# Kernel optimization log

Measured on AMD Instinct MI355X. Metric: run time of the kernel, lower is better.

Reference implementation:

```python
import jax, jax.numpy as jnp
import numpy as np

# class_mask_range after __init__ normalization: first range (-1,1) => min=-1, max=1,
# so the rescale 2*(x-min)/(max-min)-1 is the identity on all ranges.
RANGES = [(-1.0, 1.0), (-1.0, -0.5), (-0.5, 0.0), (0.0, 0.5), (0.5, 1.0)]
N_CLASSES = len(RANGES)
WEIGHTS = [1.0 / N_CLASSES] * N_CLASSES  # class_weight [1]*5 normalized by its sum


def setup_inputs() -> dict:
    key = jax.random.key(0)
    k1, k2 = jax.random.split(key)
    shape = (16, 1, 1024, 1024)
    return {
        "pre_img": jax.random.normal(k1, shape, dtype=jnp.float32),
        "real_img": jax.random.normal(k2, shape, dtype=jnp.float32),
    }


def reference(pre_img, real_img):
    # |pre*mask - real*mask| == mask * |pre - real| for 0/1 masks
    diff = jnp.abs(pre_img - real_img)
    class_mask = jnp.zeros(real_img.shape, dtype=jnp.int32)
    single_class_losses = []
    for i, (lb, ub) in enumerate(RANGES):
        m = (real_img >= lb) & (real_img <= ub)
        # later ranges overwrite earlier assignments, as in the torch loop
        class_mask = jnp.where(m, jnp.int32(i), class_mask)
        counts = m.sum()
        masked_sum = jnp.where(m, diff, 0.0).sum()
        denom = jnp.maximum(counts, 1).astype(diff.dtype)
        loss_i = jnp.where(counts == 0, 0.0, masked_sum / denom) * WEIGHTS[i]
        single_class_losses.append(loss_i)
    loss = sum(single_class_losses)
    class_mask_out = 2.0 * class_mask.astype(jnp.float32) / (N_CLASSES - 1) - 1.0
    return loss, jnp.stack(single_class_losses), class_mask_out
```

## Files before the change

### kernel.cpp

```cpp
#include <hip/hip_runtime.h>


__global__ __launch_bounds__(256) void mcl_main(
    const float* __restrict__ pre, const float* __restrict__ real,
    float* __restrict__ mask_out, float* __restrict__ sums,
    unsigned int* __restrict__ counts, int n4, int n)
{
    float s[5] = {0.f, 0.f, 0.f, 0.f, 0.f};
    unsigned int c[5] = {0u, 0u, 0u, 0u, 0u};

    const int tid = blockIdx.x * blockDim.x + threadIdx.x;
    const int stride = gridDim.x * blockDim.x;

    for (int i = tid; i < n4; i += stride) {
        float4 p = ((const float4*)pre)[i];
        float4 r = ((const float4*)real)[i];
        float pv[4] = {p.x, p.y, p.z, p.w};
        float rv[4] = {r.x, r.y, r.z, r.w};
        float ov[4];
#pragma unroll
        for (int k = 0; k < 4; ++k) {
            float rr = rv[k];
            float d = fabsf(pv[k] - rr);
            bool in0 = (rr >= -1.0f) && (rr <= 1.0f);
            bool in1 = (rr >= -1.0f) && (rr <= -0.5f);
            bool in2 = (rr >= -0.5f) && (rr <= 0.0f);
            bool in3 = (rr >= 0.0f) && (rr <= 0.5f);
            bool in4 = (rr >= 0.5f) && (rr <= 1.0f);
            s[0] += in0 ? d : 0.f; c[0] += in0;
            s[1] += in1 ? d : 0.f; c[1] += in1;
            s[2] += in2 ? d : 0.f; c[2] += in2;
            s[3] += in3 ? d : 0.f; c[3] += in3;
            s[4] += in4 ? d : 0.f; c[4] += in4;
            int cls = in4 ? 4 : (in3 ? 3 : (in2 ? 2 : (in1 ? 1 : 0)));
            ov[k] = 0.5f * (float)cls - 1.0f;
        }
        float2* mo = (float2*)(mask_out + 4 * (size_t)i);
        mo[0] = make_float2(ov[0], ov[1]);
        mo[1] = make_float2(ov[2], ov[3]);
    }

    int tail_base = n4 * 4;
    int tail = n - tail_base;
    if (tid < tail) {
        int idx = tail_base + tid;
        float rr = real[idx];
        float d = fabsf(pre[idx] - rr);
        bool in0 = (rr >= -1.0f) && (rr <= 1.0f);
        bool in1 = (rr >= -1.0f) && (rr <= -0.5f);
        bool in2 = (rr >= -0.5f) && (rr <= 0.0f);
        bool in3 = (rr >= 0.0f) && (rr <= 0.5f);
        bool in4 = (rr >= 0.5f) && (rr <= 1.0f);
        s[0] += in0 ? d : 0.f; c[0] += in0;
        s[1] += in1 ? d : 0.f; c[1] += in1;
        s[2] += in2 ? d : 0.f; c[2] += in2;
        s[3] += in3 ? d : 0.f; c[3] += in3;
        s[4] += in4 ? d : 0.f; c[4] += in4;
        int cls = in4 ? 4 : (in3 ? 3 : (in2 ? 2 : (in1 ? 1 : 0)));
        mask_out[idx] = 0.5f * (float)cls - 1.0f;
    }

#pragma unroll
    for (int j = 0; j < 5; ++j) {
#pragma unroll
        for (int off = 32; off > 0; off >>= 1) {
            s[j] += __shfl_down(s[j], off, 64);
            c[j] += __shfl_down(c[j], off, 64);
        }
    }

    __shared__ float ls[4][5];
    __shared__ unsigned int lc[4][5];
    int lane = threadIdx.x & 63;
    int wave = threadIdx.x >> 6;
    if (lane == 0) {
#pragma unroll
        for (int j = 0; j < 5; ++j) { ls[wave][j] = s[j]; lc[wave][j] = c[j]; }
    }
    __syncthreads();
    if (threadIdx.x < 5) {
        float ssum = ls[0][threadIdx.x] + ls[1][threadIdx.x]
                   + ls[2][threadIdx.x] + ls[3][threadIdx.x];
        unsigned int csum = lc[0][threadIdx.x] + lc[1][threadIdx.x]
                          + lc[2][threadIdx.x] + lc[3][threadIdx.x];
        atomicAdd(&sums[threadIdx.x], ssum);
        atomicAdd(&counts[threadIdx.x], csum);
    }
}

__global__ void mcl_final(const float* __restrict__ sums,
                          const unsigned int* __restrict__ counts,
                          float* __restrict__ out)
{
    if (threadIdx.x == 0) {
        float total = 0.f;
        float losses[5];
#pragma unroll
        for (int j = 0; j < 5; ++j) {
            unsigned int cnt = counts[j];
            unsigned int denom = cnt > 1u ? cnt : 1u;
            float l = (cnt == 0u) ? 0.f : (sums[j] / (float)denom) * 0.2f;
            losses[j] = l;
            total += l;
        }
        out[0] = total;
#pragma unroll
        for (int j = 0; j < 5; ++j) out[1 + j] = losses[j];
    }
}

extern "C" void kernel_launch(void* const* d_in, const int* in_sizes, int n_in,
                              void* d_out, int out_size, void* d_ws, size_t ws_size,
                              hipStream_t stream) {
    const float* pre  = (const float*)d_in[0];
    const float* real = (const float*)d_in[1];
    float* out = (float*)d_out;
    int n = in_sizes[0];
    int n4 = n / 4;

    float* sums = (float*)d_ws;
    unsigned int* counts = (unsigned int*)((char*)d_ws + 5 * sizeof(float));

    hipMemsetAsync(d_ws, 0, 10 * sizeof(float), stream);

    const int blocks = 1024;
    mcl_main<<<blocks, 256, 0, stream>>>(pre, real, out + 6, sums, counts, n4, n);
    mcl_final<<<1, 64, 0, stream>>>(sums, counts, out);
}
```

Baseline: 189.8 us.

## Launch one block per 512 float4s with two loads per thread and padded atomics

Replaces the fixed 1024-block grid-stride loop with a grid sized to the data, where each thread issues both of its two float4 loads up front and then processes them. The global accumulators are spread 64 slots apart so each class counter sits on its own cache line, and the launch bounds now request 8 blocks per CU. This exposes more memory-level parallelism and reduces contention on the shared atomic counters. In exchange there are far more blocks, about 8192, and so many more per-block atomics to the global accumulators.

```diff
diff --git a/kernel.cpp b/kernel.cpp
--- a/kernel.cpp
+++ b/kernel.cpp
@@ -1,7 +1,35 @@
 #include <hip/hip_runtime.h>
 
 
-__global__ __launch_bounds__(256) void mcl_main(
+#define ACC_STRIDE 64
+
+__device__ __forceinline__ void proc_elem(float pv, float rv,
+                                          float s[5], unsigned int c[5],
+                                          float& ov) {
+    float d = fabsf(pv - rv);
+    bool geM1  = rv >= -1.0f;
+    bool leM05 = rv <= -0.5f;
+    bool geM05 = rv >= -0.5f;
+    bool le0   = rv <=  0.0f;
+    bool ge0   = rv >=  0.0f;
+    bool le05  = rv <=  0.5f;
+    bool ge05  = rv >=  0.5f;
+    bool le1   = rv <=  1.0f;
+    bool in0 = geM1  && le1;
+    bool in1 = geM1  && leM05;
+    bool in2 = geM05 && le0;
+    bool in3 = ge0   && le05;
+    bool in4 = ge05  && le1;
+    s[0] += in0 ? d : 0.f;  c[0] += in0;
+    s[1] += in1 ? d : 0.f;  c[1] += in1;
+    s[2] += in2 ? d : 0.f;  c[2] += in2;
+    s[3] += in3 ? d : 0.f;  c[3] += in3;
+    s[4] += in4 ? d : 0.f;  c[4] += in4;
+    int cls = in4 ? 4 : (in3 ? 3 : (in2 ? 2 : (in1 ? 1 : 0)));
+    ov = 0.5f * (float)cls - 1.0f;
+}
+
+__global__ __launch_bounds__(256, 8) void mcl_main(
     const float* __restrict__ pre, const float* __restrict__ real,
     float* __restrict__ mask_out, float* __restrict__ sums,
     unsigned int* __restrict__ counts, int n4, int n)
@@ -9,55 +37,50 @@
     float s[5] = {0.f, 0.f, 0.f, 0.f, 0.f};
     unsigned int c[5] = {0u, 0u, 0u, 0u, 0u};
 
-    const int tid = blockIdx.x * blockDim.x + threadIdx.x;
-    const int stride = gridDim.x * blockDim.x;
+    const int t = threadIdx.x;
+    const int i0 = blockIdx.x * 512 + t;
+    const int i1 = i0 + 256;
+    const bool v0 = i0 < n4;
+    const bool v1 = i1 < n4;
 
-    for (int i = tid; i < n4; i += stride) {
-        float4 p = ((const float4*)pre)[i];
-        float4 r = ((const float4*)real)[i];
-        float pv[4] = {p.x, p.y, p.z, p.w};
-        float rv[4] = {r.x, r.y, r.z, r.w};
+    const float4* pre4  = (const float4*)pre;
+    const float4* real4 = (const float4*)real;
+
+    float4 p0, r0, p1, r1;
+    if (v0) { p0 = pre4[i0]; r0 = real4[i0]; }
+    if (v1) { p1 = pre4[i1]; r1 = real4[i1]; }
+
+    if (v0) {
         float ov[4];
-#pragma unroll
-        for (int k = 0; k < 4; ++k) {
-            float rr = rv[k];
-            float d = fabsf(pv[k] - rr);
-            bool in0 = (rr >= -1.0f) && (rr <= 1.0f);
-            bool in1 = (rr >= -1.0f) && (rr <= -0.5f);
-            bool in2 = (rr >= -0.5f) && (rr <= 0.0f);
-            bool in3 = (rr >= 0.0f) && (rr <= 0.5f);
-            bool in4 = (rr >= 0.5f) && (rr <= 1.0f);
-            s[0] += in0 ? d : 0.f; c[0] += in0;
-            s[1] += in1 ? d : 0.f; c[1] += in1;
-            s[2] += in2 ? d : 0.f; c[2] += in2;
-            s[3] += in3 ? d : 0.f; c[3] += in3;
-            s[4] += in4 ? d : 0.f; c[4] += in4;
-            int cls = in4 ? 4 : (in3 ? 3 : (in2 ? 2 : (in1 ? 1 : 0)));
-            ov[k] = 0.5f * (float)cls - 1.0f;
-        }
-        float2* mo = (float2*)(mask_out + 4 * (size_t)i);
+        proc_elem(p0.x, r0.x, s, c, ov[0]);
+        proc_elem(p0.y, r0.y, s, c, ov[1]);
+        proc_elem(p0.z, r0.z, s, c, ov[2]);
+        proc_elem(p0.w, r0.w, s, c, ov[3]);
+        float2* mo = (float2*)(mask_out + 4 * (size_t)i0);
+        mo[0] = make_float2(ov[0], ov[1]);
+        mo[1] = make_float2(ov[2], ov[3]);
+    }
+    if (v1) {
+        float ov[4];
+        proc_elem(p1.x, r1.x, s, c, ov[0]);
+        proc_elem(p1.y, r1.y, s, c, ov[1]);
+        proc_elem(p1.z, r1.z, s, c, ov[2]);
+        proc_elem(p1.w, r1.w, s, c, ov[3]);
+        float2* mo = (float2*)(mask_out + 4 * (size_t)i1);
         mo[0] = make_float2(ov[0], ov[1]);
         mo[1] = make_float2(ov[2], ov[3]);
     }
 
-    int tail_base = n4 * 4;
-    int tail = n - tail_base;
-    if (tid < tail) {
-        int idx = tail_base + tid;
-        float rr = real[idx];
-        float d = fabsf(pre[idx] - rr);
-        bool in0 = (rr >= -1.0f) && (rr <= 1.0f);
-        bool in1 = (rr >= -1.0f) && (rr <= -0.5f);
-        bool in2 = (rr >= -0.5f) && (rr <= 0.0f);
-        bool in3 = (rr >= 0.0f) && (rr <= 0.5f);
-        bool in4 = (rr >= 0.5f) && (rr <= 1.0f);
-        s[0] += in0 ? d : 0.f; c[0] += in0;
-        s[1] += in1 ? d : 0.f; c[1] += in1;
-        s[2] += in2 ? d : 0.f; c[2] += in2;
-        s[3] += in3 ? d : 0.f; c[3] += in3;
-        s[4] += in4 ? d : 0.f; c[4] += in4;
-        int cls = in4 ? 4 : (in3 ? 3 : (in2 ? 2 : (in1 ? 1 : 0)));
-        mask_out[idx] = 0.5f * (float)cls - 1.0f;
+    {
+        int tail_base = n4 * 4;
+        int tail = n - tail_base;
+        int gtid = blockIdx.x * blockDim.x + t;
+        if (gtid < tail) {
+            int idx = tail_base + gtid;
+            float ov;
+            proc_elem(pre[idx], real[idx], s, c, ov);
+            mask_out[idx] = ov;
+        }
     }
 
 #pragma unroll
@@ -71,20 +94,18 @@
 
     __shared__ float ls[4][5];
     __shared__ unsigned int lc[4][5];
-    int lane = threadIdx.x & 63;
-    int wave = threadIdx.x >> 6;
+    int lane = t & 63;
+    int wave = t >> 6;
     if (lane == 0) {
 #pragma unroll
         for (int j = 0; j < 5; ++j) { ls[wave][j] = s[j]; lc[wave][j] = c[j]; }
     }
     __syncthreads();
-    if (threadIdx.x < 5) {
-        float ssum = ls[0][threadIdx.x] + ls[1][threadIdx.x]
-                   + ls[2][threadIdx.x] + ls[3][threadIdx.x];
-        unsigned int csum = lc[0][threadIdx.x] + lc[1][threadIdx.x]
-                          + lc[2][threadIdx.x] + lc[3][threadIdx.x];
-        atomicAdd(&sums[threadIdx.x], ssum);
-        atomicAdd(&counts[threadIdx.x], csum);
+    if (t < 5) {
+        float ssum = ls[0][t] + ls[1][t] + ls[2][t] + ls[3][t];
+        unsigned int csum = lc[0][t] + lc[1][t] + lc[2][t] + lc[3][t];
+        atomicAdd(&sums[t * ACC_STRIDE], ssum);
+        atomicAdd(&counts[t * ACC_STRIDE], csum);
     }
 }
 
@@ -97,9 +118,9 @@
         float losses[5];
 #pragma unroll
         for (int j = 0; j < 5; ++j) {
-            unsigned int cnt = counts[j];
+            unsigned int cnt = counts[j * ACC_STRIDE];
             unsigned int denom = cnt > 1u ? cnt : 1u;
-            float l = (cnt == 0u) ? 0.f : (sums[j] / (float)denom) * 0.2f;
+            float l = (cnt == 0u) ? 0.f : (sums[j * ACC_STRIDE] / (float)denom) * 0.2f;
             losses[j] = l;
             total += l;
         }
@@ -119,11 +140,12 @@
     int n4 = n / 4;
 
     float* sums = (float*)d_ws;
-    unsigned int* counts = (unsigned int*)((char*)d_ws + 5 * sizeof(float));
+    unsigned int* counts = (unsigned int*)d_ws + 5 * ACC_STRIDE;
 
-    hipMemsetAsync(d_ws, 0, 10 * sizeof(float), stream);
+    hipMemsetAsync(d_ws, 0, 10 * ACC_STRIDE * sizeof(float), stream);
 
-    const int blocks = 1024;
+    int blocks = (n4 + 511) / 512;
+    if (blocks < 1) blocks = 1;
     mcl_main<<<blocks, 256, 0, stream>>>(pre, real, out + 6, sums, counts, n4, n);
     mcl_final<<<1, 64, 0, stream>>>(sums, counts, out);
 }
```

Result: slower. 237.9 us (+25.3%).
